# Kernel tuning notes

Hardware: AMD Instinct MI355X
Metric: run time of the kernel (lower is better)

Reference implementation:

```python
import jax, jax.numpy as jnp
import numpy as np

FEATURES = 1024
EXPANDED = 16
HIDDEN = FEATURES * EXPANDED  # 16384
BATCH = 4096


def setup_inputs() -> dict:
    key = jax.random.key(0)
    k_x, k_we, k_be, k_wd, k_bd = jax.random.split(key, 5)
    s_enc = 1.0 / np.sqrt(FEATURES)
    s_dec = 1.0 / np.sqrt(HIDDEN)
    return {
        "x": jax.random.normal(k_x, (BATCH, FEATURES), dtype=jnp.float32),
        "W_enc": jax.random.uniform(k_we, (HIDDEN, FEATURES), jnp.float32, -s_enc, s_enc),
        "b_enc": jax.random.uniform(k_be, (HIDDEN,), jnp.float32, -s_enc, s_enc),
        "W_dec": jax.random.uniform(k_wd, (FEATURES, HIDDEN), jnp.float32, -s_dec, s_dec),
        "b_dec": jax.random.uniform(k_bd, (FEATURES,), jnp.float32, -s_dec, s_dec),
        "activate": 64,
    }


def reference(x, W_enc, b_enc, W_dec, b_dec, activate):
    # Encoder: subtract decoder bias, dense GEMM -> pre-activations a [B, HIDDEN]
    xbar = x - b_dec
    a = jnp.einsum("bf,hf->bh", xbar, W_enc) + b_enc
    # TopK per row, relu values, scatter back into a zero tensor
    vals, idx = jax.lax.top_k(a, activate)           # [B, k]
    f = jnp.zeros_like(a)
    rows = jnp.arange(a.shape[0])[:, None]           # [B, 1]
    f = f.at[rows, idx].set(jax.nn.relu(vals))
    # Decoder: dense GEMM back to feature space (faithful to original dense decode)
    xhat = jnp.einsum("bh,fh->bf", f, W_dec) + b_dec
    return f, xhat
```

## Files before the change

kernel.cpp:

```cpp
#include <hip/hip_runtime.h>
#include <cstdint>

#define B_ 4096
#define F_ 1024
#define H_ 16384
#define TOPK 64
#define MAXC 192
#define TWOE 0.020f

typedef unsigned short u16;
typedef __attribute__((ext_vector_type(8))) _Float16 f16x8;
typedef __attribute__((ext_vector_type(8))) unsigned short u16x8;
typedef __attribute__((ext_vector_type(4))) float f32x4;

__device__ __forceinline__ u16 f2bf(float f) {
  union { float f; uint32_t u; } v; v.f = f;
  uint32_t u = v.u;
  uint32_t r = u + 0x7FFFu + ((u >> 16) & 1u);
  return (u16)(r >> 16);
}
__device__ __forceinline__ float bf2f(u16 h) {
  union { uint32_t u; float f; } v; v.u = ((uint32_t)h) << 16; return v.f;
}
__device__ __forceinline__ u16 f2h(float f) {
  union { _Float16 h; u16 u; } v; v.h = (_Float16)f; return v.u;
}
__device__ __forceinline__ float h2f(u16 h) {
  union { _Float16 h; u16 u; } v; v.u = h; return (float)v.h;
}
__device__ __forceinline__ uint32_t key2(uint32_t v) {
  uint32_t s = (v >> 15) & 0x00010001u;
  return v & ~(s * 0xFFFFu);
}

__device__ __forceinline__ void async16(const void* g, void* l) {
  __builtin_amdgcn_global_load_lds(
      reinterpret_cast<const __attribute__((address_space(1))) uint32_t*>(
          reinterpret_cast<uintptr_t>(g)),
      reinterpret_cast<__attribute__((address_space(3))) uint32_t*>(
          reinterpret_cast<uintptr_t>(l)),
      16, 0, 0);
}

__global__ __launch_bounds__(256) void k_xbar(const float* __restrict__ x,
                                              const float* __restrict__ b_dec,
                                              u16* __restrict__ xbar) {
  int i = blockIdx.x * 256 + threadIdx.x;
  int base = i * 4;
  int col = base & (F_ - 1);
  float4 xv = *(const float4*)(x + base);
  float4 bv = *(const float4*)(b_dec + col);
  ushort4 o;
  o.x = f2h(xv.x - bv.x); o.y = f2h(xv.y - bv.y);
  o.z = f2h(xv.z - bv.z); o.w = f2h(xv.w - bv.w);
  *(ushort4*)(xbar + base) = o;
}

__global__ __launch_bounds__(256) void k_cast(const float* __restrict__ src,
                                              u16* __restrict__ dst) {
  size_t base = (size_t)(blockIdx.x * 256 + threadIdx.x) * 4;
  float4 v = *(const float4*)(src + base);
  ushort4 o; o.x = f2h(v.x); o.y = f2h(v.y); o.z = f2h(v.z); o.w = f2h(v.w);
  *(ushort4*)(dst + base) = o;
}

__global__ __launch_bounds__(256) void k_transpose(const float* __restrict__ Wdec,
                                                   u16* __restrict__ WdecT) {
  __shared__ float tile[32][33];
  int hb = blockIdx.x * 32, fb = blockIdx.y * 32;
  int tx = threadIdx.x & 31, ty = threadIdx.x >> 5;
#pragma unroll
  for (int i = 0; i < 32; i += 8)
    tile[ty + i][tx] = Wdec[(size_t)(fb + ty + i) * H_ + hb + tx];
  __syncthreads();
#pragma unroll
  for (int i = 0; i < 32; i += 8)
    WdecT[(size_t)(hb + ty + i) * F_ + fb + tx] = f2bf(tile[tx][ty + i]);
}

__global__ __launch_bounds__(256) void k_gemm(const u16* __restrict__ A,
                                              const u16* __restrict__ Bm,
                                              const float* __restrict__ b_enc,
                                              u16* __restrict__ Cf16,
                                              float* __restrict__ fzero) {
  __shared__ u16 lA[128 * 32];
  __shared__ u16 lB[128 * 32];
  const int tid = threadIdx.x;
  const int lane = tid & 63, wave = tid >> 6;
  const int wm = wave >> 1, wn = wave & 1;
  const int bx = blockIdx.x, by = blockIdx.y;

  const int kcs = (tid & 3) ^ ((tid >> 3) & 3);
  const u16* gA0 = A + (size_t)(by * 128 + (tid >> 2)) * F_ + kcs * 8;
  const u16* gB0 = Bm + (size_t)(bx * 128 + (tid >> 2)) * F_ + kcs * 8;
  u16* lA0 = &lA[tid * 8];
  u16* lB0 = &lB[tid * 8];

  f32x4 acc[4][4] = {};
  const int lm = lane & 15;
  const int kcp = (((lane >> 4) ^ ((lm >> 1) & 3))) * 8;

  for (int k0 = 0; k0 < F_; k0 += 32) {
    async16(gA0 + k0, lA0);
    async16(gA0 + 64 * F_ + k0, lA0 + 2048);
    async16(gB0 + k0, lB0);
    async16(gB0 + 64 * F_ + k0, lB0 + 2048);
    __syncthreads();
    f16x8 av[4], bv[4];
#pragma unroll
    for (int i = 0; i < 4; ++i)
      av[i] = *(const f16x8*)&lA[(wm * 64 + i * 16 + lm) * 32 + kcp];
#pragma unroll
    for (int j = 0; j < 4; ++j)
      bv[j] = *(const f16x8*)&lB[(wn * 64 + j * 16 + lm) * 32 + kcp];
#pragma unroll
    for (int i = 0; i < 4; ++i)
#pragma unroll
      for (int j = 0; j < 4; ++j)
        acc[i][j] = __builtin_amdgcn_mfma_f32_16x16x32_f16(av[i], bv[j], acc[i][j], 0, 0, 0);
    __syncthreads();
  }

  {
    const int bid = by * gridDim.x + bx;
    float* zp = fzero + (size_t)bid * 8192 + tid * 4;
    const f32x4 z4 = {0.f, 0.f, 0.f, 0.f};
#pragma unroll
    for (int k = 0; k < 8; ++k)
      __builtin_nontemporal_store(z4, (f32x4*)(zp + k * 1024));
  }

#pragma unroll
  for (int i = 0; i < 4; ++i) {
    int rowg = by * 128 + wm * 64 + i * 16 + (lane >> 4) * 4;
#pragma unroll
    for (int j = 0; j < 4; ++j) {
      int colg = bx * 128 + wn * 64 + j * 16 + lm;
      float be = b_enc[colg];
      u16* cp = Cf16 + (size_t)rowg * H_ + colg;
#pragma unroll
      for (int r = 0; r < 4; ++r)
        cp[(size_t)r * H_] = f2h(acc[i][j][r] + be);
    }
  }
}

__global__ __launch_bounds__(256) void k_selref(const u16* __restrict__ af16,
                                                const float* __restrict__ x,
                                                const float* __restrict__ b_dec,
                                                const float* __restrict__ Wenc,
                                                const float* __restrict__ b_enc,
                                                int* __restrict__ decIdx,
                                                float* __restrict__ decVal) {
  const int row = blockIdx.x, tid = threadIdx.x;
  const int lane = tid & 63, wave = tid >> 6;
  __shared__ float wbuf[4][2][F_];
  __shared__ float xs[F_];
  __shared__ double vals[MAXC];
  __shared__ float bes[MAXC];
  __shared__ int idxs[MAXC];
  __shared__ int s_cnt4[4];
  __shared__ int s_sure, s_amb;

  if (tid == 0) { s_sure = 0; s_amb = 0; idxs[0] = 0; }
  for (int k = tid; k < F_; k += 256)
    xs[k] = x[(size_t)row * F_ + k] - b_dec[k];

  uint32_t pr[32];
  {
    const uint4* arow16 = (const uint4*)(af16 + (size_t)row * H_);
#pragma unroll
    for (int j = 0; j < 8; ++j) {
      uint4 v = arow16[tid + 256 * j];
      pr[j * 4 + 0] = key2(v.x);
      pr[j * 4 + 1] = key2(v.y);
      pr[j * 4 + 2] = key2(v.z);
      pr[j * 4 + 3] = key2(v.w);
    }
  }

  uint32_t lo = 0, hi = 0x7C00;
  while (hi - lo > 1) {
    const uint32_t mid = (lo + hi) >> 1;
    int c = 0;
#pragma unroll
    for (int r = 0; r < 32; ++r) {
      c += ((pr[r] & 0xFFFFu) >= mid);
      c += ((pr[r] >> 16) >= mid);
    }
#pragma unroll
    for (int off = 32; off > 0; off >>= 1) c += __shfl_xor(c, off);
    if (lane == 0) s_cnt4[wave] = c;
    __syncthreads();
    const int tot = s_cnt4[0] + s_cnt4[1] + s_cnt4[2] + s_cnt4[3];
    if (tot >= TOPK) lo = mid; else hi = mid;
    __syncthreads();
  }
  const float v64f = h2f((u16)lo);
  const float sc = v64f + TWOE;
  const float al = v64f - TWOE;

  int* dI = decIdx + row * TOPK;
  float* dV = decVal + row * TOPK;
#pragma unroll
  for (int j = 0; j < 8; ++j) {
#pragma unroll
    for (int w = 0; w < 4; ++w) {
      const uint32_t v = pr[j * 4 + w];
      const int ib = (tid + 256 * j) * 8 + w * 2;
      const float f0 = h2f((u16)(v & 0xFFFFu));
      const float f1 = h2f((u16)(v >> 16));
      if (f0 > sc) {
        int p = atomicAdd(&s_sure, 1);
        if (p < TOPK) { dI[p] = ib; dV[p] = f0 > 0.f ? f0 : 0.f; }
      } else if (f0 >= al) {
        int p = atomicAdd(&s_amb, 1);
        if (p < MAXC) idxs[p] = ib;
      }
      if (f1 > sc) {
        int p = atomicAdd(&s_sure, 1);
        if (p < TOPK) { dI[p] = ib + 1; dV[p] = f1 > 0.f ? f1 : 0.f; }
      } else if (f1 >= al) {
        int p = atomicAdd(&s_amb, 1);
        if (p < MAXC) idxs[p] = ib + 1;
      }
    }
  }
  __syncthreads();
  const int S = s_sure < TOPK ? s_sure : TOPK;
  const int cnt = s_amb < MAXC ? s_amb : MAXC;
  for (int c = tid; c < cnt; c += 256) bes[c] = b_enc[idxs[c]];
  __syncthreads();

  float xr[16];
#pragma unroll
  for (int ch = 0; ch < 4; ++ch)
#pragma unroll
    for (int j = 0; j < 4; ++j)
      xr[ch * 4 + j] = xs[ch * 256 + lane * 4 + j];

#define ISSUE_ROW(c_, b_)                                                  \
  {                                                                        \
    int cc_ = (c_) < cnt ? (c_) : 0;                                       \
    const float* src_ = Wenc + (size_t)idxs[cc_] * F_ + lane * 4;          \
    float* dst_ = &wbuf[wave][(b_)][lane * 4];                             \
    async16(src_ + 0, dst_ + 0);                                           \
    async16(src_ + 256, dst_ + 256);                                       \
    async16(src_ + 512, dst_ + 512);                                       \
    async16(src_ + 768, dst_ + 768);                                       \
  }

  const int nIter = (cnt - wave + 3) / 4;
  ISSUE_ROW(wave, 0);
  ISSUE_ROW(wave + 4, 1);

  for (int i = 0; i < nIter; ++i) {
    const int c = wave + i * 4;
    const int bsel = i & 1;
    asm volatile("s_waitcnt vmcnt(4)" ::: "memory");
    __builtin_amdgcn_sched_barrier(0);

    const float4* wr = (const float4*)wbuf[wave][bsel];
    double s = 0.0;
#pragma unroll
    for (int ch = 0; ch < 4; ++ch) {
      float4 wv = wr[ch * 64 + lane];
      s = fma((double)xr[ch * 4 + 0], (double)wv.x, s);
      s = fma((double)xr[ch * 4 + 1], (double)wv.y, s);
      s = fma((double)xr[ch * 4 + 2], (double)wv.z, s);
      s = fma((double)xr[ch * 4 + 3], (double)wv.w, s);
    }
    __builtin_amdgcn_sched_barrier(0);
    ISSUE_ROW(wave + (i + 2) * 4, bsel);

#pragma unroll
    for (int off = 32; off > 0; off >>= 1) s += __shfl_xor(s, off);
    if (lane == 0 && c < cnt) vals[c] = s + (double)bes[c];
  }
#undef ISSUE_ROW
  __syncthreads();

  const int Kp = TOPK - S;
  for (int c = tid; c < cnt; c += 256) {
    const double v = vals[c];
    const int h = idxs[c];
    int rank = 0;
    for (int o = 0; o < cnt; ++o) {
      double vo = vals[o];
      rank += (vo > v) || (vo == v && idxs[o] < h);
    }
    if (rank < Kp) {
      float fv = v > 0.0 ? (float)v : 0.0f;
      dI[S + rank] = h;
      dV[S + rank] = fv;
    }
  }
}

__global__ __launch_bounds__(256) void k_decode(const int* __restrict__ decIdx,
                                               const float* __restrict__ decVal,
                                               const u16* __restrict__ WdecT,
                                               const float* __restrict__ b_dec,
                                               float* __restrict__ f,
                                               float* __restrict__ xhat) {
  const int row = blockIdx.x, tid = threadIdx.x;
  __shared__ int sIdx[TOPK];
  __shared__ float sVal[TOPK];
  if (tid < TOPK) {
    sIdx[tid] = decIdx[row * TOPK + tid] & (H_ - 1);
    sVal[tid] = decVal[row * TOPK + tid];
  }
  float* frow = f + (size_t)row * H_;
  if (row >= B_ / 2) {
    const f32x4 z4 = {0.f, 0.f, 0.f, 0.f};
    for (int i = tid; i < H_ / 4; i += 256)
      __builtin_nontemporal_store(z4, (f32x4*)frow + i);
  }
  __syncthreads();
  if (tid < TOPK) frow[sIdx[tid]] = sVal[tid];

  const int fb = tid * 4;
  float4 bd = *(const float4*)(b_dec + fb);
  float a0 = bd.x, a1 = bd.y, a2 = bd.z, a3 = bd.w;
#pragma unroll 8
  for (int j = 0; j < TOPK; ++j) {
    const float v = sVal[j];
    const ushort4 w = *(const ushort4*)(WdecT + (size_t)sIdx[j] * F_ + fb);
    a0 += v * bf2f(w.x); a1 += v * bf2f(w.y);
    a2 += v * bf2f(w.z); a3 += v * bf2f(w.w);
  }
  float4 o; o.x = a0; o.y = a1; o.z = a2; o.w = a3;
  *(float4*)(xhat + (size_t)row * F_ + fb) = o;
}

extern "C" void kernel_launch(void* const* d_in, const int* in_sizes, int n_in,
                              void* d_out, int out_size, void* d_ws, size_t ws_size,
                              hipStream_t stream) {
  const float* x    = (const float*)d_in[0];
  const float* Wenc = (const float*)d_in[1];
  const float* benc = (const float*)d_in[2];
  const float* Wdec = (const float*)d_in[3];
  const float* bdec = (const float*)d_in[4];

  float* out  = (float*)d_out;
  float* f    = out;
  float* xhat = out + (size_t)B_ * H_;
  u16* af16 = (u16*)(f + (size_t)B_ * H_ / 2);

  char* ws = (char*)d_ws;
  u16*  xbar    = (u16*)ws;
  u16*  wencb   = (u16*)(ws + (size_t)(8)  * 1048576);
  u16*  wdecT   = (u16*)(ws + (size_t)(40) * 1048576);
  int*  decIdx  = (int*)(ws + (size_t)(76) * 1048576);
  float* decVal = (float*)(ws + (size_t)(77) * 1048576);

  k_xbar<<<B_ * F_ / 1024, 256, 0, stream>>>(x, bdec, xbar);
  k_cast<<<H_ * F_ / 1024, 256, 0, stream>>>(Wenc, wencb);
  k_transpose<<<dim3(H_ / 32, F_ / 32), 256, 0, stream>>>(Wdec, wdecT);
  k_gemm<<<dim3(H_ / 128, B_ / 128), 256, 0, stream>>>(xbar, wencb, benc, af16, f);
  k_selref<<<B_, 256, 0, stream>>>(af16, x, bdec, Wenc, benc, decIdx, decVal);
  k_decode<<<B_, 256, 0, stream>>>(decIdx, decVal, wdecT, bdec, f, xhat);
}
```

Before: 743.8 us.

## Double-buffer encoder GEMM LDS, trim selection barriers, split decode reduction

The encoder GEMM now uses two LDS buffers, so the async global-to-LDS copy of the next K slice is issued while MFMAs run on the current one, with one barrier per step instead of two. The GEMM is launched as two half-batch grids. The top-k threshold search alternates between two shared count buffers, which drops one barrier per bisection step. The decoder splits the 64 nonzeros across two thread halves that load 8-wide and combine partial sums through shared memory. The extra LDS buffer lowers GEMM occupancy, and the second launch adds overhead.

New measurement: 747.8 us. No clear change (+0.5%).

```diff
diff --git a/kernel.cpp b/kernel.cpp
--- a/kernel.cpp
+++ b/kernel.cpp
@@ -78,51 +78,69 @@
     WdecT[(size_t)(hb + ty + i) * F_ + fb + tx] = f2bf(tile[tx][ty + i]);
 }
 
+__device__ __forceinline__ void gemm_step(const u16* __restrict__ bA,
+                                          const u16* __restrict__ bB,
+                                          int aoff, int boff, int kcp,
+                                          f32x4 (&acc)[4][4]) {
+  f16x8 av[4], bv[4];
+#pragma unroll
+  for (int i = 0; i < 4; ++i)
+    av[i] = *(const f16x8*)&bA[(aoff + i * 16) * 32 + kcp];
+#pragma unroll
+  for (int j = 0; j < 4; ++j)
+    bv[j] = *(const f16x8*)&bB[(boff + j * 16) * 32 + kcp];
+#pragma unroll
+  for (int i = 0; i < 4; ++i)
+#pragma unroll
+    for (int j = 0; j < 4; ++j)
+      acc[i][j] = __builtin_amdgcn_mfma_f32_16x16x32_f16(av[i], bv[j], acc[i][j], 0, 0, 0);
+}
+
 __global__ __launch_bounds__(256) void k_gemm(const u16* __restrict__ A,
                                               const u16* __restrict__ Bm,
                                               const float* __restrict__ b_enc,
                                               u16* __restrict__ Cf16,
-                                              float* __restrict__ fzero) {
-  __shared__ u16 lA[128 * 32];
-  __shared__ u16 lB[128 * 32];
+                                              float* __restrict__ fzero,
+                                              int by0) {
+  __shared__ u16 lA[2][128 * 32];
+  __shared__ u16 lB[2][128 * 32];
   const int tid = threadIdx.x;
   const int lane = tid & 63, wave = tid >> 6;
   const int wm = wave >> 1, wn = wave & 1;
-  const int bx = blockIdx.x, by = blockIdx.y;
+  const int bx = blockIdx.x, by = by0 + blockIdx.y;
 
   const int kcs = (tid & 3) ^ ((tid >> 3) & 3);
   const u16* gA0 = A + (size_t)(by * 128 + (tid >> 2)) * F_ + kcs * 8;
   const u16* gB0 = Bm + (size_t)(bx * 128 + (tid >> 2)) * F_ + kcs * 8;
-  u16* lA0 = &lA[tid * 8];
-  u16* lB0 = &lB[tid * 8];
+
+#define STAGE(b_, k0_)                                       \
+  {                                                          \
+    async16(gA0 + (k0_), &lA[b_][tid * 8]);                  \
+    async16(gA0 + 64 * F_ + (k0_), &lA[b_][tid * 8 + 2048]); \
+    async16(gB0 + (k0_), &lB[b_][tid * 8]);                  \
+    async16(gB0 + 64 * F_ + (k0_), &lB[b_][tid * 8 + 2048]); \
+  }
 
   f32x4 acc[4][4] = {};
   const int lm = lane & 15;
   const int kcp = (((lane >> 4) ^ ((lm >> 1) & 3))) * 8;
-
-  for (int k0 = 0; k0 < F_; k0 += 32) {
-    async16(gA0 + k0, lA0);
-    async16(gA0 + 64 * F_ + k0, lA0 + 2048);
-    async16(gB0 + k0, lB0);
-    async16(gB0 + 64 * F_ + k0, lB0 + 2048);
+  const int aoff = wm * 64 + lm, boff = wn * 64 + lm;
+
+  STAGE(0, 0);
+  __syncthreads();
+  int cur = 0;
+#pragma unroll 1
+  for (int t = 0; t < 31; ++t) {
+    STAGE(cur ^ 1, (t + 1) * 32);
+    gemm_step(lA[cur], lB[cur], aoff, boff, kcp, acc);
     __syncthreads();
-    f16x8 av[4], bv[4];
-#pragma unroll
-    for (int i = 0; i < 4; ++i)
-      av[i] = *(const f16x8*)&lA[(wm * 64 + i * 16 + lm) * 32 + kcp];
-#pragma unroll
-    for (int j = 0; j < 4; ++j)
-      bv[j] = *(const f16x8*)&lB[(wn * 64 + j * 16 + lm) * 32 + kcp];
-#pragma unroll
-    for (int i = 0; i < 4; ++i)
-#pragma unroll
-      for (int j = 0; j < 4; ++j)
-        acc[i][j] = __builtin_amdgcn_mfma_f32_16x16x32_f16(av[i], bv[j], acc[i][j], 0, 0, 0);
-    __syncthreads();
-  }
+    cur ^= 1;
+  }
+  gemm_step(lA[cur], lB[cur], aoff, boff, kcp, acc);
+#undef STAGE
 
   {
-    const int bid = by * gridDim.x + bx;
+    const int bid = by * 128 + bx;
     float* zp = fzero + (size_t)bid * 8192 + tid * 4;
     const f32x4 z4 = {0.f, 0.f, 0.f, 0.f};
 #pragma unroll
@@ -159,7 +177,7 @@
   __shared__ double vals[MAXC];
   __shared__ float bes[MAXC];
   __shared__ int idxs[MAXC];
-  __shared__ int s_cnt4[4];
+  __shared__ int s_cnt8[2][4];
   __shared__ int s_sure, s_amb;
 
   if (tid == 0) { s_sure = 0; s_amb = 0; idxs[0] = 0; }
@@ -180,6 +198,7 @@
   }
 
   uint32_t lo = 0, hi = 0x7C00;
+  int it = 0;
   while (hi - lo > 1) {
     const uint32_t mid = (lo + hi) >> 1;
     int c = 0;
@@ -190,11 +209,12 @@
     }
 #pragma unroll
     for (int off = 32; off > 0; off >>= 1) c += __shfl_xor(c, off);
-    if (lane == 0) s_cnt4[wave] = c;
+    if (lane == 0) s_cnt8[it & 1][wave] = c;
     __syncthreads();
-    const int tot = s_cnt4[0] + s_cnt4[1] + s_cnt4[2] + s_cnt4[3];
+    const int* sc = s_cnt8[it & 1];
+    const int tot = sc[0] + sc[1] + sc[2] + sc[3];
     if (tot >= TOPK) lo = mid; else hi = mid;
-    __syncthreads();
+    ++it;
   }
   const float v64f = h2f((u16)lo);
   const float sc = v64f + TWOE;
@@ -306,6 +326,7 @@
   const int row = blockIdx.x, tid = threadIdx.x;
   __shared__ int sIdx[TOPK];
   __shared__ float sVal[TOPK];
+  __shared__ float part[F_];
   if (tid < TOPK) {
     sIdx[tid] = decIdx[row * TOPK + tid] & (H_ - 1);
     sVal[tid] = decVal[row * TOPK + tid];
@@ -319,18 +340,38 @@
   __syncthreads();
   if (tid < TOPK) frow[sIdx[tid]] = sVal[tid];
 
-  const int fb = tid * 4;
-  float4 bd = *(const float4*)(b_dec + fb);
-  float a0 = bd.x, a1 = bd.y, a2 = bd.z, a3 = bd.w;
+  const int cb = (tid & 127) * 8;
+  const int par = tid >> 7;
+  float a[8] = {0.f, 0.f, 0.f, 0.f, 0.f, 0.f, 0.f, 0.f};
 #pragma unroll 8
-  for (int j = 0; j < TOPK; ++j) {
+  for (int j2 = 0; j2 < TOPK / 2; ++j2) {
+    const int j = j2 * 2 + par;
     const float v = sVal[j];
-    const ushort4 w = *(const ushort4*)(WdecT + (size_t)sIdx[j] * F_ + fb);
-    a0 += v * bf2f(w.x); a1 += v * bf2f(w.y);
-    a2 += v * bf2f(w.z); a3 += v * bf2f(w.w);
-  }
-  float4 o; o.x = a0; o.y = a1; o.z = a2; o.w = a3;
-  *(float4*)(xhat + (size_t)row * F_ + fb) = o;
+    const u16x8 w = *(const u16x8*)(WdecT + (size_t)sIdx[j] * F_ + cb);
+#pragma unroll
+    for (int k = 0; k < 8; ++k) a[k] += v * bf2f(w[k]);
+  }
+  if (par) {
+#pragma unroll
+    for (int k = 0; k < 8; ++k) part[cb + k] = a[k];
+  }
+  __syncthreads();
+  if (!par) {
+    float4 bd0 = *(const float4*)(b_dec + cb);
+    float4 bd1 = *(const float4*)(b_dec + cb + 4);
+    float4 o0, o1;
+    o0.x = a[0] + part[cb + 0] + bd0.x;
+    o0.y = a[1] + part[cb + 1] + bd0.y;
+    o0.z = a[2] + part[cb + 2] + bd0.z;
+    o0.w = a[3] + part[cb + 3] + bd0.w;
+    o1.x = a[4] + part[cb + 4] + bd1.x;
+    o1.y = a[5] + part[cb + 5] + bd1.y;
+    o1.z = a[6] + part[cb + 6] + bd1.z;
+    o1.w = a[7] + part[cb + 7] + bd1.w;
+    float* xp = xhat + (size_t)row * F_ + cb;
+    *(float4*)xp = o0;
+    *(float4*)(xp + 4) = o1;
+  }
 }
 
 extern "C" void kernel_launch(void* const* d_in, const int* in_sizes, int n_in,
@@ -357,7 +398,8 @@
   k_xbar<<<B_ * F_ / 1024, 256, 0, stream>>>(x, bdec, xbar);
   k_cast<<<H_ * F_ / 1024, 256, 0, stream>>>(Wenc, wencb);
   k_transpose<<<dim3(H_ / 32, F_ / 32), 256, 0, stream>>>(Wdec, wdecT);
-  k_gemm<<<dim3(H_ / 128, B_ / 128), 256, 0, stream>>>(xbar, wencb, benc, af16, f);
+  k_gemm<<<dim3(H_ / 128, B_ / 256), 256, 0, stream>>>(xbar, wencb, benc, af16, f, 0);
+  k_gemm<<<dim3(H_ / 128, B_ / 256), 256, 0, stream>>>(xbar, wencb, benc, af16, f, 16);
   k_selref<<<B_, 256, 0, stream>>>(af16, x, bdec, Wenc, benc, decIdx, decVal);
   k_decode<<<B_, 256, 0, stream>>>(decIdx, decVal, wdecT, bdec, f, xhat);
 }
```
